# Optimization experiments

Hardware: AMD Instinct MI355X
Metric: run time of the kernel (lower is better)

The kernel has to match this reference:

```python
import jax, jax.numpy as jnp
import numpy as np

RADIUS = 5  # kernels_radius -> diameter 11, 121 window taps
KERNELS_DESC = [
    {"weight": 0.9, "xy": 6.0, "rgb": 0.1},  # RGBXY kernel
    {"weight": 0.1, "xy": 6.0},               # XY kernel
]


def _unfold(img, r):
    # img: [N, C, H, W] -> [N, C, d, d, H, W] with zero padding (== F.unfold semantics)
    N, C, H, W = img.shape
    d = 2 * r + 1
    p = jnp.pad(img, ((0, 0), (0, 0), (r, r), (r, r)))
    patches = jnp.stack(
        [p[:, :, dy:dy + H, dx:dx + W] for dy in range(d) for dx in range(d)], axis=2
    )
    return patches.reshape(N, C, d, d, H, W)


def _get_mesh(N, H, W, dtype):
    xs = jnp.broadcast_to(jnp.arange(W, dtype=dtype).reshape(1, 1, 1, W), (N, 1, H, W))
    ys = jnp.broadcast_to(jnp.arange(H, dtype=dtype).reshape(1, 1, H, 1), (N, 1, H, W))
    return jnp.concatenate((xs, ys), axis=1)  # [N, 2, H, W]


def _kernel_from_features(features, r):
    # features: [N, C, H, W] -> Gaussian affinity [N, 1, d, d, H, W], center zeroed
    N, C, H, W = features.shape
    k = _unfold(features, r)                         # [N, C, d, d, H, W]
    center = k[:, :, r, r, :, :][:, :, None, None]   # [N, C, 1, 1, H, W]
    k = jnp.exp(jnp.sum(-0.5 * (k - center) ** 2, axis=1, keepdims=True))
    k = k.at[:, :, r, r, :, :].set(0.0)
    return k


def _forward(y_hat_softmax, rgb):
    N, C, H, W = y_hat_softmax.shape
    # adaptive_avg_pool2d 256->128 is an exact 2x2 mean pool
    _, Cr, Hi, Wi = rgb.shape
    rgb_ds = rgb.reshape(N, Cr, H, Hi // H, W, Wi // W).mean(axis=(3, 5))
    mesh = _get_mesh(N, H, W, y_hat_softmax.dtype)

    kernels = None
    for desc in KERNELS_DESC:
        feats = []
        for modality, sigma in desc.items():
            if modality == "weight":
                continue
            f = mesh if modality == "xy" else rgb_ds
            feats.append(f / jnp.asarray(sigma, y_hat_softmax.dtype))
        features = jnp.concatenate(feats, axis=1)
        k = desc["weight"] * _kernel_from_features(features, RADIUS)
        kernels = k if kernels is None else kernels + k

    denom = N * H * W
    d = 2 * RADIUS + 1
    y_unf = _unfold(y_hat_softmax, RADIUS)                       # [N, C, d, d, H, W]
    prod = (kernels * y_unf).reshape(N, C, d * d, H, W).sum(axis=2)  # [N, C, H, W]
    loss = kernels.sum() - (prod * y_hat_softmax).sum()
    return loss / denom


def setup_inputs() -> dict:
    key = jax.random.key(0)
    k1, k2 = jax.random.split(key)
    logits = jax.random.normal(k1, (2, 21, 128, 128), dtype=jnp.float32)
    y_hat_softmax = jax.nn.softmax(logits, axis=1)
    rgb = jax.random.uniform(k2, (2, 3, 256, 256), dtype=jnp.float32)
    return {"y_hat_softmax": y_hat_softmax, "rgb": rgb}


def reference(y_hat_softmax, rgb):
    return _forward(y_hat_softmax, rgb)
```

## Files before the change

### kernel.cpp

```cpp
#include <hip/hip_runtime.h>

#define RAD   5
#define DIA   11
#define IMH   128
#define IMW   128
#define NCH   21
#define TILE  8
#define SW    18
#define SP    324
#define NBLK  512

__global__ __launch_bounds__(256)
void crf_partial(const float* __restrict__ y, const float* __restrict__ rgb,
                 float* __restrict__ ws) {
    __shared__ float4 ys4[SP * 7];
    __shared__ float2 fxy[SP];
    __shared__ float  wtab[128];
    __shared__ int    otab[128];
    __shared__ float  wred[4];

    const int tid = threadIdx.x;
    const int b   = blockIdx.x;
    const int tx0 = (b & 15) * TILE;
    const int ty0 = ((b >> 4) & 15) * TILE;
    const int n   = b >> 8;
    const int x0  = tx0 - RAD, y0 = ty0 - RAD;
    const bool interior = (x0 >= 0) & (y0 >= 0) & (x0 + SW <= IMW) & (y0 + SW <= IMH);

    if (tid < 121) {
        int dy = tid / DIA, dx = tid - dy * DIA;
        float ddx = (dx - RAD) * (1.0f / 6.0f);
        float ddy = (dy - RAD) * (1.0f / 6.0f);
        wtab[tid] = (tid == 60) ? 0.0f : __expf(-0.5f * (ddx * ddx + ddy * ddy));
        otab[tid] = (dy - RAD) * SW + (dx - RAD);
    }

    for (int i = tid; i < SP; i += 256) {
        int sy = i / SW, sx = i - sy * SW;
        int gx = x0 + sx, gy = y0 + sy;
        float fx = 0.f, fy = 0.f;
        if (gx >= 0 && gx < IMW && gy >= 0 && gy < IMH) {
            fx = (float)gx * (1.0f / 6.0f);
            fy = (float)gy * (1.0f / 6.0f);
        }
        fxy[i] = make_float2(fx, fy);
    }

    for (int i = tid; i < SP * 6; i += 256) {
        int cg4 = i / SP, px = i - cg4 * SP;
        int sy = px / SW, sx = px - sy * SW;
        int gx = x0 + sx, gy = y0 + sy;
        float4 v = make_float4(0.f, 0.f, 0.f, 0.f);
        if (gx >= 0 && gx < IMW && gy >= 0 && gy < IMH) {
            const float* yp = y + ((n * NCH) << 14) + (gy << 7) + gx;
            if (cg4 < 5) {
                int c0 = cg4 * 4;
                v.x = yp[(c0 + 0) << 14];
                v.y = yp[(c0 + 1) << 14];
                v.z = yp[(c0 + 2) << 14];
                v.w = yp[(c0 + 3) << 14];
            } else {
                v.x = yp[20 << 14];
                const int cs = 256 * 256;
                const float* rp = rgb + ((n * 3) * cs + (gy << 9) + (gx << 1));
                v.y = (rp[0]      + rp[1]        + rp[256]      + rp[257])      * 2.5f;
                v.z = (rp[cs]     + rp[cs + 1]   + rp[cs + 256] + rp[cs + 257]) * 2.5f;
                v.w = (rp[2*cs]   + rp[2*cs + 1] + rp[2*cs+256] + rp[2*cs+257]) * 2.5f;
            }
        }
        ys4[px * 7 + cg4] = v;
    }
    __syncthreads();

    const int px  = tid & 63;
    const int grp = tid >> 6;
    const int lx  = px & 7, ly = px >> 3;
    const int ci  = (ly + RAD) * SW + (lx + RAD);

    const float4* ycp = ys4 + ci * 7;
    const float4 c0 = ycp[0], c1 = ycp[1], c2 = ycp[2],
                 c3 = ycp[3], c4 = ycp[4], c5 = ycp[5];
    const float2 cf = fxy[ci];

    float acc = 0.f;
    if (interior) {
        for (int t = grp; t < 121; t += 4) {
            const int nb = ci + otab[t];
            const float4* yn = ys4 + nb * 7;
            const float4 a0 = yn[0], a1 = yn[1], a2 = yn[2],
                         a3 = yn[3], a4 = yn[4], a5 = yn[5];
            const float dr = c5.y - a5.y, dg = c5.z - a5.z, db = c5.w - a5.w;
            const float K  = wtab[t] * (0.9f * __expf(-0.5f * (dr*dr + dg*dg + db*db)) + 0.1f);
            float dot;
            dot  = a0.x * c0.x + a0.y * c0.y + a0.z * c0.z + a0.w * c0.w;
            dot += a1.x * c1.x + a1.y * c1.y + a1.z * c1.z + a1.w * c1.w;
            dot += a2.x * c2.x + a2.y * c2.y + a2.z * c2.z + a2.w * c2.w;
            dot += a3.x * c3.x + a3.y * c3.y + a3.z * c3.z + a3.w * c3.w;
            dot += a4.x * c4.x + a4.y * c4.y + a4.z * c4.z + a4.w * c4.w;
            dot += a5.x * c5.x;
            acc += K * (1.0f - dot);
        }
    } else {
        for (int t = grp; t < 121; t += 4) {
            const int nb = ci + otab[t];
            const float4* yn = ys4 + nb * 7;
            const float2 nf = fxy[nb];
            const float4 a0 = yn[0], a1 = yn[1], a2 = yn[2],
                         a3 = yn[3], a4 = yn[4], a5 = yn[5];
            const float dfx = cf.x - nf.x, dfy = cf.y - nf.y;
            const float dr  = c5.y - a5.y, dg = c5.z - a5.z, db = c5.w - a5.w;
            float K = __expf(-0.5f * (dfx*dfx + dfy*dfy)) *
                      (0.9f * __expf(-0.5f * (dr*dr + dg*dg + db*db)) + 0.1f);
            K = (t == 60) ? 0.0f : K;
            float dot;
            dot  = a0.x * c0.x + a0.y * c0.y + a0.z * c0.z + a0.w * c0.w;
            dot += a1.x * c1.x + a1.y * c1.y + a1.z * c1.z + a1.w * c1.w;
            dot += a2.x * c2.x + a2.y * c2.y + a2.z * c2.z + a2.w * c2.w;
            dot += a3.x * c3.x + a3.y * c3.y + a3.z * c3.z + a3.w * c3.w;
            dot += a4.x * c4.x + a4.y * c4.y + a4.z * c4.z + a4.w * c4.w;
            dot += a5.x * c5.x;
            acc += K * (1.0f - dot);
        }
    }

    for (int off = 32; off > 0; off >>= 1) acc += __shfl_down(acc, off);
    if ((tid & 63) == 0) wred[tid >> 6] = acc;
    __syncthreads();
    if (tid == 0) ws[b] = wred[0] + wred[1] + wred[2] + wred[3];
}

__global__ __launch_bounds__(256)
void crf_finalize(const float* __restrict__ ws, float* __restrict__ out) {
    __shared__ float wred[4];
    const int tid = threadIdx.x;
    float v = ws[tid] + ws[tid + 256];
    for (int off = 32; off > 0; off >>= 1) v += __shfl_down(v, off);
    if ((tid & 63) == 0) wred[tid >> 6] = v;
    __syncthreads();
    if (tid == 0) out[0] = (wred[0] + wred[1] + wred[2] + wred[3]) * (1.0f / 32768.0f);
}

extern "C" void kernel_launch(void* const* d_in, const int* in_sizes, int n_in,
                              void* d_out, int out_size, void* d_ws, size_t ws_size,
                              hipStream_t stream) {
    const float* y   = (const float*)d_in[0];
    const float* rgb = (const float*)d_in[1];
    float* out = (float*)d_out;
    float* ws  = (float*)d_ws;

    crf_partial<<<dim3(NBLK), dim3(256), 0, stream>>>(y, rgb, ws);
    crf_finalize<<<dim3(1), dim3(256), 0, stream>>>(ws, out);
}
```

Baseline: 72.03 us.

## Exploit pairwise kernel symmetry and pack probabilities as fp16 with dot2

Interior tiles now visit only the first half of the 121 window taps and double the result, relying on the pairwise term K(p,q)(1 - y_p·y_q) being symmetric. Boundary tiles still visit every tap but weight each one by neighbour validity, so the global sum is unchanged. The 21 class probabilities are stored in shared memory as packed fp16 pairs and multiplied with the amdgcn fdot2 intrinsic. RGB features stay fp32, and the staging loads are merged into one pass per pixel. This cuts tap work and shared-memory traffic roughly in half, at the cost of fp16 rounding in the dot product.

New measurement: 70.18 us. 2.6% less time.

```diff
diff --git a/kernel.cpp b/kernel.cpp
--- a/kernel.cpp
+++ b/kernel.cpp
@@ -9,11 +9,31 @@
 #define SW    18
 #define SP    324
 #define NBLK  512
+#define PSTR  5
+
+typedef _Float16 half2_t __attribute__((ext_vector_type(2)));
+
+__device__ __forceinline__ float fdot2(unsigned a, unsigned b, float acc) {
+#if __has_builtin(__builtin_amdgcn_fdot2)
+    return __builtin_amdgcn_fdot2(__builtin_bit_cast(half2_t, a),
+                                  __builtin_bit_cast(half2_t, b), acc, false);
+#else
+    half2_t ha = __builtin_bit_cast(half2_t, a);
+    half2_t hb = __builtin_bit_cast(half2_t, b);
+    return acc + (float)ha[0] * (float)hb[0] + (float)ha[1] * (float)hb[1];
+#endif
+}
+
+__device__ __forceinline__ unsigned pack2(float x, float y) {
+    unsigned short lo = __builtin_bit_cast(unsigned short, (_Float16)x);
+    unsigned short hi = __builtin_bit_cast(unsigned short, (_Float16)y);
+    return (unsigned)lo | ((unsigned)hi << 16);
+}
 
 __global__ __launch_bounds__(256)
 void crf_partial(const float* __restrict__ y, const float* __restrict__ rgb,
                  float* __restrict__ ws) {
-    __shared__ float4 ys4[SP * 7];
+    __shared__ uint4  tile[SP * PSTR];
     __shared__ float2 fxy[SP];
     __shared__ float  wtab[128];
     __shared__ int    otab[128];
@@ -38,37 +58,31 @@
     for (int i = tid; i < SP; i += 256) {
         int sy = i / SW, sx = i - sy * SW;
         int gx = x0 + sx, gy = y0 + sy;
-        float fx = 0.f, fy = 0.f;
-        if (gx >= 0 && gx < IMW && gy >= 0 && gy < IMH) {
-            fx = (float)gx * (1.0f / 6.0f);
-            fy = (float)gy * (1.0f / 6.0f);
-        }
-        fxy[i] = make_float2(fx, fy);
-    }
-
-    for (int i = tid; i < SP * 6; i += 256) {
-        int cg4 = i / SP, px = i - cg4 * SP;
-        int sy = px / SW, sx = px - sy * SW;
-        int gx = x0 + sx, gy = y0 + sy;
-        float4 v = make_float4(0.f, 0.f, 0.f, 0.f);
+        uint4 q0 = make_uint4(0, 0, 0, 0), q1 = q0, q2 = q0, q3 = q0;
+        float2 f = make_float2(0.f, 0.f);
         if (gx >= 0 && gx < IMW && gy >= 0 && gy < IMH) {
             const float* yp = y + ((n * NCH) << 14) + (gy << 7) + gx;
-            if (cg4 < 5) {
-                int c0 = cg4 * 4;
-                v.x = yp[(c0 + 0) << 14];
-                v.y = yp[(c0 + 1) << 14];
-                v.z = yp[(c0 + 2) << 14];
-                v.w = yp[(c0 + 3) << 14];
-            } else {
-                v.x = yp[20 << 14];
-                const int cs = 256 * 256;
-                const float* rp = rgb + ((n * 3) * cs + (gy << 9) + (gx << 1));
-                v.y = (rp[0]      + rp[1]        + rp[256]      + rp[257])      * 2.5f;
-                v.z = (rp[cs]     + rp[cs + 1]   + rp[cs + 256] + rp[cs + 257]) * 2.5f;
-                v.w = (rp[2*cs]   + rp[2*cs + 1] + rp[2*cs+256] + rp[2*cs+257]) * 2.5f;
-            }
+            float c[NCH];
+            #pragma unroll
+            for (int ch = 0; ch < NCH; ++ch) c[ch] = yp[ch << 14];
+            q0 = make_uint4(pack2(c[0], c[1]),   pack2(c[2], c[3]),
+                            pack2(c[4], c[5]),   pack2(c[6], c[7]));
+            q1 = make_uint4(pack2(c[8], c[9]),   pack2(c[10], c[11]),
+                            pack2(c[12], c[13]), pack2(c[14], c[15]));
+            q2 = make_uint4(pack2(c[16], c[17]), pack2(c[18], c[19]),
+                            pack2(c[20], 0.f),   __float_as_uint(1.0f));
+            const int cs = 256 * 256;
+            const float* rp = rgb + (n * 3) * cs + (gy << 9) + (gx << 1);
+            float r  = (rp[0]      + rp[1]        + rp[256]      + rp[257])      * 2.5f;
+            float g  = (rp[cs]     + rp[cs + 1]   + rp[cs + 256] + rp[cs + 257]) * 2.5f;
+            float bl = (rp[2*cs]   + rp[2*cs + 1] + rp[2*cs+256] + rp[2*cs+257]) * 2.5f;
+            q3 = make_uint4(__float_as_uint(r), __float_as_uint(g),
+                            __float_as_uint(bl), 0);
+            f = make_float2((float)gx * (1.0f / 6.0f), (float)gy * (1.0f / 6.0f));
         }
-        ys4[px * 7 + cg4] = v;
+        uint4* tp = tile + i * PSTR;
+        tp[0] = q0; tp[1] = q1; tp[2] = q2; tp[3] = q3;
+        fxy[i] = f;
     }
     __syncthreads();
 
@@ -77,49 +91,55 @@
     const int lx  = px & 7, ly = px >> 3;
     const int ci  = (ly + RAD) * SW + (lx + RAD);
 
-    const float4* ycp = ys4 + ci * 7;
-    const float4 c0 = ycp[0], c1 = ycp[1], c2 = ycp[2],
-                 c3 = ycp[3], c4 = ycp[4], c5 = ycp[5];
+    const uint4* cp = tile + ci * PSTR;
+    const uint4 c0 = cp[0], c1 = cp[1], c2 = cp[2], c3 = cp[3];
+    const float cr = __uint_as_float(c3.x), cg = __uint_as_float(c3.y),
+                cb = __uint_as_float(c3.z);
     const float2 cf = fxy[ci];
 
     float acc = 0.f;
     if (interior) {
-        for (int t = grp; t < 121; t += 4) {
+        for (int t = grp; t < 60; t += 4) {
             const int nb = ci + otab[t];
-            const float4* yn = ys4 + nb * 7;
-            const float4 a0 = yn[0], a1 = yn[1], a2 = yn[2],
-                         a3 = yn[3], a4 = yn[4], a5 = yn[5];
-            const float dr = c5.y - a5.y, dg = c5.z - a5.z, db = c5.w - a5.w;
-            const float K  = wtab[t] * (0.9f * __expf(-0.5f * (dr*dr + dg*dg + db*db)) + 0.1f);
-            float dot;
-            dot  = a0.x * c0.x + a0.y * c0.y + a0.z * c0.z + a0.w * c0.w;
-            dot += a1.x * c1.x + a1.y * c1.y + a1.z * c1.z + a1.w * c1.w;
-            dot += a2.x * c2.x + a2.y * c2.y + a2.z * c2.z + a2.w * c2.w;
-            dot += a3.x * c3.x + a3.y * c3.y + a3.z * c3.z + a3.w * c3.w;
-            dot += a4.x * c4.x + a4.y * c4.y + a4.z * c4.z + a4.w * c4.w;
-            dot += a5.x * c5.x;
+            const uint4* p = tile + nb * PSTR;
+            const uint4 a0 = p[0], a1 = p[1], a2 = p[2], a3 = p[3];
+            float dot = 0.f;
+            dot = fdot2(a0.x, c0.x, dot); dot = fdot2(a0.y, c0.y, dot);
+            dot = fdot2(a0.z, c0.z, dot); dot = fdot2(a0.w, c0.w, dot);
+            dot = fdot2(a1.x, c1.x, dot); dot = fdot2(a1.y, c1.y, dot);
+            dot = fdot2(a1.z, c1.z, dot); dot = fdot2(a1.w, c1.w, dot);
+            dot = fdot2(a2.x, c2.x, dot); dot = fdot2(a2.y, c2.y, dot);
+            dot = fdot2(a2.z, c2.z, dot);
+            const float dr = cr - __uint_as_float(a3.x);
+            const float dg = cg - __uint_as_float(a3.y);
+            const float db = cb - __uint_as_float(a3.z);
+            const float K  = wtab[t] *
+                (0.9f * __expf(-0.5f * (dr*dr + dg*dg + db*db)) + 0.1f);
             acc += K * (1.0f - dot);
         }
+        acc += acc;
     } else {
         for (int t = grp; t < 121; t += 4) {
             const int nb = ci + otab[t];
-            const float4* yn = ys4 + nb * 7;
+            const uint4* p = tile + nb * PSTR;
+            const uint4 a0 = p[0], a1 = p[1], a2 = p[2], a3 = p[3];
             const float2 nf = fxy[nb];
-            const float4 a0 = yn[0], a1 = yn[1], a2 = yn[2],
-                         a3 = yn[3], a4 = yn[4], a5 = yn[5];
+            float dot = 0.f;
+            dot = fdot2(a0.x, c0.x, dot); dot = fdot2(a0.y, c0.y, dot);
+            dot = fdot2(a0.z, c0.z, dot); dot = fdot2(a0.w, c0.w, dot);
+            dot = fdot2(a1.x, c1.x, dot); dot = fdot2(a1.y, c1.y, dot);
+            dot = fdot2(a1.z, c1.z, dot); dot = fdot2(a1.w, c1.w, dot);
+            dot = fdot2(a2.x, c2.x, dot); dot = fdot2(a2.y, c2.y, dot);
+            dot = fdot2(a2.z, c2.z, dot);
             const float dfx = cf.x - nf.x, dfy = cf.y - nf.y;
-            const float dr  = c5.y - a5.y, dg = c5.z - a5.z, db = c5.w - a5.w;
-            float K = __expf(-0.5f * (dfx*dfx + dfy*dfy)) *
-                      (0.9f * __expf(-0.5f * (dr*dr + dg*dg + db*db)) + 0.1f);
-            K = (t == 60) ? 0.0f : K;
-            float dot;
-            dot  = a0.x * c0.x + a0.y * c0.y + a0.z * c0.z + a0.w * c0.w;
-            dot += a1.x * c1.x + a1.y * c1.y + a1.z * c1.z + a1.w * c1.w;
-            dot += a2.x * c2.x + a2.y * c2.y + a2.z * c2.z + a2.w * c2.w;
-            dot += a3.x * c3.x + a3.y * c3.y + a3.z * c3.z + a3.w * c3.w;
-            dot += a4.x * c4.x + a4.y * c4.y + a4.z * c4.z + a4.w * c4.w;
-            dot += a5.x * c5.x;
-            acc += K * (1.0f - dot);
+            const float dr  = cr - __uint_as_float(a3.x);
+            const float dg  = cg - __uint_as_float(a3.y);
+            const float db  = cb - __uint_as_float(a3.z);
+            const float K = __expf(-0.5f * (dfx*dfx + dfy*dfy)) *
+                            (0.9f * __expf(-0.5f * (dr*dr + dg*dg + db*db)) + 0.1f);
+            const bool vld = (a2.w != 0u);
+            const float w = (t < 60) ? (vld ? 2.0f : 1.0f) : (vld ? 0.0f : 1.0f);
+            acc += w * K * (1.0f - dot);
         }
     }
 
```
